# Performance work log

Measured on AMD Instinct MI355X. Metric: run time of the kernel, lower is better.

The kernel has to match this reference:

```python
import jax, jax.numpy as jnp
import numpy as np


def setup_inputs() -> dict:
    key = jax.random.key(0)
    ks = jax.random.split(key, 8)
    B, S, H = 2, 2048, 2048
    Hq, Hkv, D = 16, 4, H // 16
    s = 0.02
    return {
        "query": jax.random.normal(ks[0], (B, S, H), jnp.float32),
        "key": jax.random.normal(ks[1], (B, S, H), jnp.float32),
        "value": jax.random.normal(ks[2], (B, S, H), jnp.float32),
        "Wq": jax.random.normal(ks[3], (H, Hq * D), jnp.float32) * s,
        "bq": jnp.zeros((Hq * D,), jnp.float32),
        "Wk": jax.random.normal(ks[4], (H, Hkv * D), jnp.float32) * s,
        "bk": jnp.zeros((Hkv * D,), jnp.float32),
        "Wv": jax.random.normal(ks[5], (H, Hkv * D), jnp.float32) * s,
        "bv": jnp.zeros((Hkv * D,), jnp.float32),
        "Wo": jax.random.normal(ks[6], (H, H), jnp.float32) * s,
        "bo": jnp.zeros((H,), jnp.float32),
    }


def reference(query, key, value, Wq, bq, Wk, bk, Wv, bv, Wo, bo):
    Hq, Hkv = 16, 4
    B, S, H = query.shape
    D = H // Hq
    G = Hq // Hkv  # heads per KV group
    # projections
    q = query @ Wq + bq   # [B,S,Hq*D]
    k = key @ Wk + bk     # [B,S,Hkv*D]
    v = value @ Wv + bv   # [B,S,Hkv*D]
    # [B, Hkv(groups), G(heads per group), S, D] for q; [B, Hkv, S, D] for k,v
    q = q.reshape(B, S, Hkv, G, D).transpose(0, 2, 3, 1, 4)
    k = k.reshape(B, S, Hkv, D).transpose(0, 2, 1, 3)
    v = v.reshape(B, S, Hkv, D).transpose(0, 2, 1, 3)
    # NOTE: original module applies NO 1/sqrt(D) scaling -- kept faithful.
    attn = jnp.einsum('bghqd,bgkd->bghqk', q, k)  # [B,Hkv,G,S,S]
    attn = jax.nn.softmax(attn, axis=-1)
    out = jnp.einsum('bghqk,bgkd->bghqd', attn, v)  # [B,Hkv,G,S,D]
    # permute(0,3,1,2,4) -> [B,S,Hkv,G,D] -> [B,S,H]
    out = out.transpose(0, 3, 1, 2, 4).reshape(B, S, H)
    return out @ Wo + bo
```

## Files before the change

kernel.cpp:

```cpp
#include <hip/hip_runtime.h>
#include <hip/hip_bf16.h>
#include <type_traits>
#include <stdint.h>

typedef short bf16x8 __attribute__((ext_vector_type(8)));
typedef short short4v __attribute__((ext_vector_type(4)));
typedef float f32x4 __attribute__((ext_vector_type(4)));
typedef float f32x16 __attribute__((ext_vector_type(16)));

#define GLL16(gp, lp) __builtin_amdgcn_global_load_lds( \
    (const __attribute__((address_space(1))) void*)(gp), \
    (__attribute__((address_space(3))) void*)(lp), 16, 0, 0)

__device__ inline short f2bf(float f) {
    union { float f; uint32_t u; } v;
    v.f = f;
    uint32_t r = (v.u + 0x7FFFu + ((v.u >> 16) & 1u)) >> 16;
    return (short)(uint16_t)r;
}

__device__ inline bf16x8 cvt8(const float4& a, const float4& b) {
    bf16x8 o;
    o[0] = f2bf(a.x); o[1] = f2bf(a.y); o[2] = f2bf(a.z); o[3] = f2bf(a.w);
    o[4] = f2bf(b.x); o[5] = f2bf(b.y); o[6] = f2bf(b.z); o[7] = f2bf(b.w);
    return o;
}

__device__ inline uint32_t cvtpk(float lo, float hi) {
    uint32_t r;
    asm("v_cvt_pk_bf16_f32 %0, %1, %2" : "=v"(r) : "v"(lo), "v"(hi));
    return r;
}

__device__ inline bf16x8 mk8(uint32_t a, uint32_t b, uint32_t c, uint32_t d) {
    union { uint32_t u[4]; bf16x8 v; } t;
    t.u[0] = a; t.u[1] = b; t.u[2] = c; t.u[3] = d;
    return t.v;
}

__device__ inline void xchg_pf(const uint32_t c[8], bool hib, bf16x8& fA, bf16x8& fB) {
    uint32_t p0 = (uint32_t)__shfl_xor((int)c[0], 32);
    uint32_t p1 = (uint32_t)__shfl_xor((int)c[1], 32);
    uint32_t p2 = (uint32_t)__shfl_xor((int)c[2], 32);
    uint32_t p3 = (uint32_t)__shfl_xor((int)c[3], 32);
    fA = mk8(hib ? p2 : c[0], hib ? p3 : c[1], hib ? c[2] : p0, hib ? c[3] : p1);
    uint32_t p4 = (uint32_t)__shfl_xor((int)c[4], 32);
    uint32_t p5 = (uint32_t)__shfl_xor((int)c[5], 32);
    uint32_t p6 = (uint32_t)__shfl_xor((int)c[6], 32);
    uint32_t p7 = (uint32_t)__shfl_xor((int)c[7], 32);
    fB = mk8(hib ? p6 : c[4], hib ? p7 : c[5], hib ? c[6] : p4, hib ? c[7] : p5);
}

__global__ __launch_bounds__(256) void prep(
    const float* __restrict__ Wq, const float* __restrict__ Wk,
    const float* __restrict__ Wv, const float* __restrict__ Wo,
    short* __restrict__ WqT, short* __restrict__ WkT,
    short* __restrict__ WvT, short* __restrict__ WoT,
    const float* __restrict__ q, const float* __restrict__ k, const float* __restrict__ v,
    short* __restrict__ Xq, short* __restrict__ Xk, short* __restrict__ Xv)
{
    __shared__ short Tt[64][65];
    const int K = 2048;
    int bid = blockIdx.x;
    int t = threadIdx.x;
    if (bid < 2560) {
        const float* W; short* T; int N; int l;
        if (bid < 1024)      { W = Wq; T = WqT; N = 2048; l = bid; }
        else if (bid < 1280) { W = Wk; T = WkT; N = 512;  l = bid - 1024; }
        else if (bid < 1536) { W = Wv; T = WvT; N = 512;  l = bid - 1280; }
        else                 { W = Wo; T = WoT; N = 2048; l = bid - 1536; }
        int nt = N >> 6;
        int n0 = (l % nt) * 64, k0 = (l / nt) * 64;
        int kl = t >> 2, nb = (t & 3) * 16;
        const float* wp = W + (size_t)(k0 + kl) * N + n0 + nb;
        #pragma unroll
        for (int j = 0; j < 16; ++j) Tt[nb + j][kl] = f2bf(wp[j]);
        __syncthreads();
        int nl = t >> 2, kb = (t & 3) * 16;
        short* op = T + (size_t)(n0 + nl) * K + k0 + kb;
        #pragma unroll
        for (int j = 0; j < 16; ++j) op[j] = Tt[nl][kb + j];
    } else {
        size_t tid = (size_t)(bid - 2560) * 256 + t;
        #pragma unroll
        for (int it = 0; it < 2; ++it) {
            size_t i = tid + (size_t)it * 524288;
            const float4* p;
            p = (const float4*)(q + i * 8);
            *(bf16x8*)(Xq + i * 8) = cvt8(p[0], p[1]);
            p = (const float4*)(k + i * 8);
            *(bf16x8*)(Xk + i * 8) = cvt8(p[0], p[1]);
            p = (const float4*)(v + i * 8);
            *(bf16x8*)(Xv + i * 8) = cvt8(p[0], p[1]);
        }
    }
}

__global__ __launch_bounds__(256) void cvtk(const float* __restrict__ in,
                                            short* __restrict__ out, int n8)
{
    int i = blockIdx.x * blockDim.x + threadIdx.x;
    int stride = gridDim.x * blockDim.x;
    for (; i < n8; i += stride) {
        const float4* p = (const float4*)(in + (size_t)i * 8);
        *(bf16x8*)(out + (size_t)i * 8) = cvt8(p[0], p[1]);
    }
}

__global__ __launch_bounds__(256) void transW4(
    const float* __restrict__ W0, const float* __restrict__ W1,
    const float* __restrict__ W2, const float* __restrict__ W3,
    short* __restrict__ T0, short* __restrict__ T1,
    short* __restrict__ T2, short* __restrict__ T3)
{
    const int K = 2048;
    const float* W; short* T; int N;
    int z = blockIdx.z;
    if (z == 0)      { W = W0; T = T0; N = 2048; }
    else if (z == 1) { W = W1; T = T1; N = 512; }
    else if (z == 2) { W = W2; T = T2; N = 512; }
    else             { W = W3; T = T3; N = 2048; }
    int n0 = blockIdx.x * 64, k0 = blockIdx.y * 64;
    if (n0 >= N) return;
    __shared__ short Tt[64][65];
    int t = threadIdx.x;
    int kl = t >> 2, nb = (t & 3) * 16;
    const float* wp = W + (size_t)(k0 + kl) * N + n0 + nb;
    #pragma unroll
    for (int j = 0; j < 16; ++j) Tt[nb + j][kl] = f2bf(wp[j]);
    __syncthreads();
    int nl = t >> 2, kb = (t & 3) * 16;
    short* op = T + (size_t)(n0 + nl) * K + k0 + kb;
    #pragma unroll
    for (int j = 0; j < 16; ++j) op[j] = Tt[nl][kb + j];
}

__global__ __launch_bounds__(256) void transV(const short* __restrict__ Vb,
                                              short* __restrict__ Vt)
{
    __shared__ short T[64][65];
    int s0 = blockIdx.x * 64, d0 = blockIdx.y * 64, bg = blockIdx.z;
    int b = bg >> 2, g = bg & 3;
    int t = threadIdx.x;
    int sl = t >> 2, db = (t & 3) * 16;
    const short* vp = Vb + (size_t)(b * 2048 + s0 + sl) * 512 + g * 128 + d0 + db;
    #pragma unroll
    for (int j = 0; j < 16; ++j) T[db + j][sl] = vp[j];
    __syncthreads();
    int dl = t >> 2, sb = (t & 3) * 16;
    short* op = Vt + (size_t)(bg * 128 + d0 + dl) * 2048 + s0 + sb;
    #pragma unroll
    for (int j = 0; j < 16; ++j) op[j] = T[dl][sb + j];
}

template <typename TC>
__device__ __forceinline__ void gemm_core(
    const short* __restrict__ A, const short* __restrict__ BT,
    const float* __restrict__ bias, TC* __restrict__ C,
    int N, int K, int m0, int n0, short* As, short* Bs, int epi)
{
    const int t = threadIdx.x, w = t >> 6, lane = t & 63;
    const int lr = lane & 15, lg = lane >> 4;
    const int wm = (w >> 1) * 64, wn = (w & 1) * 64;
    f32x4 acc[4][4] = {};

    const int lrow = lane >> 3;
    const int lcg = (lane & 7) ^ (lrow & 7);
    const int sw = lr & 7;

    const short* abase[2]; const short* bbase[2];
    #pragma unroll
    for (int kc = 0; kc < 2; ++kc) {
        abase[kc] = &As[(wm + lr) * 64 + (((kc * 4 + lg) ^ sw) * 8)];
        bbase[kc] = &Bs[(wn + lr) * 64 + (((kc * 4 + lg) ^ sw) * 8)];
    }
    const short* asrc = A  + (size_t)(m0 + w * 32 + lrow) * K + lcg * 8;
    const short* bsrc = BT + (size_t)(n0 + w * 32 + lrow) * K + lcg * 8;
    short* adst = &As[(w * 32) * 64];
    short* bdst = &Bs[(w * 32) * 64];

    for (int kk = 0; kk < K; kk += 64) {
        __syncthreads();
        #pragma unroll
        for (int i = 0; i < 4; ++i) {
            GLL16(asrc + (size_t)i * 8 * K, adst + i * 512);
            GLL16(bsrc + (size_t)i * 8 * K, bdst + i * 512);
        }
        asrc += 64; bsrc += 64;
        __syncthreads();
        #pragma unroll
        for (int kc = 0; kc < 2; ++kc) {
            bf16x8 af[4], bfr[4];
            #pragma unroll
            for (int i = 0; i < 4; ++i) af[i] = *(const bf16x8*)(abase[kc] + i * 1024);
            #pragma unroll
            for (int j = 0; j < 4; ++j) bfr[j] = *(const bf16x8*)(bbase[kc] + j * 1024);
            #pragma unroll
            for (int i = 0; i < 4; ++i)
                #pragma unroll
                for (int j = 0; j < 4; ++j)
                    acc[i][j] = __builtin_amdgcn_mfma_f32_16x16x32_bf16(af[i], bfr[j], acc[i][j], 0, 0, 0);
        }
    }

    if constexpr (std::is_same<TC, short>::value) {
        if (epi == 1) {
            #pragma unroll
            for (int i = 0; i < 4; ++i) {
                #pragma unroll
                for (int j = 0; j < 4; ++j) {
                    int row = m0 + wm + i * 16 + lg * 4;
                    int col = n0 + wn + j * 16 + lr;
                    short4v s4;
                    #pragma unroll
                    for (int r = 0; r < 4; ++r) s4[r] = f2bf(acc[i][j][r] + bias[col]);
                    int bb = row >> 11, ss = row & 2047;
                    *(short4v*)((short*)C + ((size_t)(bb * 4 + (col >> 7)) * 128 + (col & 127)) * 2048 + ss) = s4;
                }
            }
            return;
        }
    }
    #pragma unroll
    for (int i = 0; i < 4; ++i) {
        #pragma unroll
        for (int j = 0; j < 4; ++j) {
            #pragma unroll
            for (int r = 0; r < 4; ++r) {
                int row = m0 + wm + i * 16 + lg * 4 + r;
                int col = n0 + wn + j * 16 + lr;
                float v = acc[i][j][r] + bias[col];
                if constexpr (std::is_same<TC, short>::value)
                    C[(size_t)row * N + col] = f2bf(v);
                else
                    C[(size_t)row * N + col] = v;
            }
        }
    }
}

template <typename TC>
__global__ __launch_bounds__(256) void gemm_std(
    const short* __restrict__ A, const short* __restrict__ BT,
    const float* __restrict__ bias, TC* __restrict__ C, int N, int K)
{
    __shared__ short As[128 * 64];
    __shared__ short Bs[128 * 64];
    int bid = blockIdx.x;
    int chunk = gridDim.x >> 3;
    int wg = (bid & 7) * chunk + (bid >> 3);
    int m0 = (wg & 31) * 128, n0 = (wg >> 5) * 128;
    gemm_core<TC>(A, BT, bias, C, N, K, m0, n0, As, Bs, 0);
}

__global__ __launch_bounds__(256) void gemm_qkv(
    const short* __restrict__ Xq, const short* __restrict__ Xk, const short* __restrict__ Xv,
    const short* __restrict__ WqT, const short* __restrict__ WkT, const short* __restrict__ WvT,
    const float* __restrict__ bq, const float* __restrict__ bk, const float* __restrict__ bv,
    short* __restrict__ Qb, short* __restrict__ Kb, short* __restrict__ Vt)
{
    __shared__ short As[128 * 64];
    __shared__ short Bs[128 * 64];
    int bid = blockIdx.x;
    int wg = (bid & 7) * 96 + (bid >> 3);
    const short* A; const short* BT; const float* bi; short* C; int N; int l; int epi;
    if (wg < 512)      { l = wg;       A = Xq; BT = WqT; bi = bq; C = Qb; N = 2048; epi = 0; }
    else if (wg < 640) { l = wg - 512; A = Xk; BT = WkT; bi = bk; C = Kb; N = 512;  epi = 0; }
    else               { l = wg - 640; A = Xv; BT = WvT; bi = bv; C = Vt; N = 512;  epi = 1; }
    int m0 = (l & 31) * 128, n0 = (l >> 5) * 128;
    gemm_core<short>(A, BT, bi, C, N, 2048, m0, n0, As, Bs, epi);
}

__global__ __launch_bounds__(512, 2) void attn_kernel(
    const short* __restrict__ Qb, const short* __restrict__ Kb,
    const short* __restrict__ Vt, short* __restrict__ Ob)
{
    const int S = 2048;
    __shared__ short Ks[2 * 64 * 128];
    __shared__ short Vs[2 * 128 * 64];

    int bid = blockIdx.x;
    int wg = (bid & 7) * 32 + (bid >> 3);
    const int qt = wg & 7, bh = wg >> 3;
    const int b = bh >> 4, h = bh & 15, g = h >> 2, bg = b * 4 + g;

    const int t = threadIdx.x, w = t >> 6, lane = t & 63;
    const int l5 = lane & 31, hi = lane >> 5;
    const bool hib = hi != 0;
    const int qg = b * S + qt * 256 + w * 32 + l5;
    const float C = 1.44269504089f;

    const short* qrow = Qb + (size_t)qg * 2048 + h * 128 + hi * 8;
    bf16x8 qf[8];
    #pragma unroll
    for (int dm = 0; dm < 8; ++dm)
        qf[dm] = *(const bf16x8*)(qrow + dm * 16);

    f32x16 o[4] = {};
    float m = -1e30f, l = 0.0f;

    const int sr4 = lane >> 4, sc4 = lane & 15;
    const int sr8 = lane >> 3, sc8 = lane & 7;
    const short* ksrc[2]; const short* vsrc[2];
    #pragma unroll
    for (int i = 0; i < 2; ++i) {
        int kr = w * 8 + i * 4 + sr4;
        ksrc[i] = Kb + (size_t)(b * S + kr) * 512 + g * 128 + ((sc4 ^ (kr & 15)) * 8);
        int d = w * 16 + i * 8 + sr8;
        vsrc[i] = Vt + (size_t)(bg * 128 + d) * 2048 + ((sc8 ^ (d & 7)) * 8);
    }

    int kx[8];
    #pragma unroll
    for (int dm = 0; dm < 8; ++dm)
        kx[dm] = (((dm * 2 + hi) ^ (l5 & 15)) * 8);
    int va[4];
    #pragma unroll
    for (int j = 0; j < 4; ++j)
        va[j] = (((2 * j + hi) ^ (l5 & 7)) * 8);

    #define STAGE(BUF, KVI) do { \
        short* kd = Ks + (BUF) * 8192 + (w * 8) * 128; \
        short* vd = Vs + (BUF) * 8192 + (w * 16) * 64; \
        size_t ko = (size_t)(KVI) * 64 * 512; \
        int vo = (KVI) * 64; \
        _Pragma("unroll") \
        for (int i = 0; i < 2; ++i) { \
            GLL16(ksrc[i] + ko, kd + i * 512); \
            GLL16(vsrc[i] + vo, vd + i * 512); \
        } \
    } while (0)

    STAGE(0, 0);
    const int NT = S / 64;
    for (int ti = 0; ti < NT; ++ti) {
        int cur = ti & 1;
        __syncthreads();
        if (ti + 1 < NT) STAGE(cur ^ 1, ti + 1);

        const short* KB = Ks + cur * 8192 + l5 * 128;
        f32x16 p0 = {}, p1 = {};
        __builtin_amdgcn_s_setprio(1);
        #pragma unroll
        for (int dm = 0; dm < 8; ++dm) {
            bf16x8 k0 = *(const bf16x8*)(KB + kx[dm]);
            bf16x8 k1 = *(const bf16x8*)(KB + 4096 + kx[dm]);
            p0 = __builtin_amdgcn_mfma_f32_32x32x16_bf16(k0, qf[dm], p0, 0, 0, 0);
            p1 = __builtin_amdgcn_mfma_f32_32x32x16_bf16(k1, qf[dm], p1, 0, 0, 0);
        }
        __builtin_amdgcn_s_setprio(0);

        float mx = -1e30f;
        #pragma unroll
        for (int e = 0; e < 16; ++e) mx = fmaxf(mx, fmaxf(p0[e], p1[e]));
        mx = fmaxf(mx, __shfl_xor(mx, 32));
        if (__any(mx > m)) {
            float mn = fmaxf(m, mx);
            float sf = exp2f((m - mn) * C);
            m = mn; l *= sf;
            #pragma unroll
            for (int dblk = 0; dblk < 4; ++dblk)
                #pragma unroll
                for (int e = 0; e < 16; ++e) o[dblk][e] *= sf;
        }
        float nmc = -m * C;
        #pragma unroll
        for (int e = 0; e < 16; ++e) {
            p0[e] = exp2f(fmaf(p0[e], C, nmc));
            p1[e] = exp2f(fmaf(p1[e], C, nmc));
        }
        float rs = 0.0f;
        #pragma unroll
        for (int e = 0; e < 16; ++e) rs += p0[e] + p1[e];
        rs += __shfl_xor(rs, 32);
        l += rs;

        uint32_t c0[8], c1[8];
        #pragma unroll
        for (int i = 0; i < 8; ++i) {
            c0[i] = cvtpk(p0[2 * i], p0[2 * i + 1]);
            c1[i] = cvtpk(p1[2 * i], p1[2 * i + 1]);
        }
        bf16x8 pf[4];
        xchg_pf(c0, hib, pf[0], pf[1]);
        xchg_pf(c1, hib, pf[2], pf[3]);

        const short* VB = Vs + cur * 8192 + l5 * 64;
        __builtin_amdgcn_s_setprio(1);
        #pragma unroll
        for (int dblk = 0; dblk < 4; ++dblk) {
            const short* vb = VB + dblk * 2048;
            #pragma unroll
            for (int j = 0; j < 4; ++j) {
                bf16x8 vf = *(const bf16x8*)(vb + va[j]);
                o[dblk] = __builtin_amdgcn_mfma_f32_32x32x16_bf16(vf, pf[j], o[dblk], 0, 0, 0);
            }
        }
        __builtin_amdgcn_s_setprio(0);
    }
    #undef STAGE

    float inv = 1.0f / l;
    short* op = Ob + (size_t)qg * 2048 + h * 128 + hi * 4;
    #pragma unroll
    for (int dblk = 0; dblk < 4; ++dblk) {
        #pragma unroll
        for (int mm = 0; mm < 4; ++mm) {
            short4v s4;
            #pragma unroll
            for (int e = 0; e < 4; ++e) s4[e] = f2bf(o[dblk][mm * 4 + e] * inv);
            *(short4v*)(op + dblk * 32 + mm * 8) = s4;
        }
    }
}

extern "C" void kernel_launch(void* const* d_in, const int* in_sizes, int n_in,
                              void* d_out, int out_size, void* d_ws, size_t ws_size,
                              hipStream_t stream)
{
    const float* query = (const float*)d_in[0];
    const float* key   = (const float*)d_in[1];
    const float* value = (const float*)d_in[2];
    const float* Wq    = (const float*)d_in[3];
    const float* bq    = (const float*)d_in[4];
    const float* Wk    = (const float*)d_in[5];
    const float* bk    = (const float*)d_in[6];
    const float* Wv    = (const float*)d_in[7];
    const float* bv    = (const float*)d_in[8];
    const float* Wo    = (const float*)d_in[9];
    const float* bo    = (const float*)d_in[10];
    float* out = (float*)d_out;

    const int BS = 4096;
    char* ws = (char*)d_ws;
    dim3 blk(256);
    const size_t MB = 1048576;

    if (ws_size >= 96 * MB) {
        short* Xq  = (short*)(ws + 0);
        short* Xk  = (short*)(ws + 16 * MB);
        short* Xv  = (short*)(ws + 32 * MB);
        short* Qb  = (short*)(ws + 48 * MB);
        short* Kb  = (short*)(ws + 64 * MB);
        short* Vtg = (short*)(ws + 72 * MB);
        short* WqT = (short*)(ws + 76 * MB);
        short* WkT = (short*)(ws + 84 * MB);
        short* WvT = (short*)(ws + 86 * MB);
        short* WoT = (short*)(ws + 88 * MB);
        short* Ob  = Xq;

        prep<<<4608, blk, 0, stream>>>(Wq, Wk, Wv, Wo, WqT, WkT, WvT, WoT,
                                       query, key, value, Xq, Xk, Xv);
        gemm_qkv<<<768, blk, 0, stream>>>(Xq, Xk, Xv, WqT, WkT, WvT, bq, bk, bv, Qb, Kb, Vtg);
        attn_kernel<<<256, dim3(512), 0, stream>>>(Qb, Kb, Vtg, Ob);
        gemm_std<float><<<512, blk, 0, stream>>>(Ob, WoT, bo, out, 2048, 2048);
    } else {
        short* Qb  = (short*)(ws + 0);
        short* Kb  = (short*)(ws + 16777216);
        short* Vb  = (short*)(ws + 20971520);
        short* Vtg = (short*)(ws + 25165824);
        short* WqT = (short*)(ws + 29360128);
        short* WkT = (short*)(ws + 37748736);
        short* WvT = (short*)(ws + 39845888);
        short* WoT = (short*)(ws + 41943040);
        short* Xbf = (short*)(ws + 50331648);

        transW4<<<dim3(32, 32, 4), blk, 0, stream>>>(Wq, Wk, Wv, Wo, WqT, WkT, WvT, WoT);
        cvtk<<<2048, blk, 0, stream>>>(query, Xbf, BS * 2048 / 8);
        gemm_std<short><<<512, blk, 0, stream>>>(Xbf, WqT, bq, Qb, 2048, 2048);
        cvtk<<<2048, blk, 0, stream>>>(key, Xbf, BS * 2048 / 8);
        gemm_std<short><<<128, blk, 0, stream>>>(Xbf, WkT, bk, Kb, 512, 2048);
        cvtk<<<2048, blk, 0, stream>>>(value, Xbf, BS * 2048 / 8);
        gemm_std<short><<<128, blk, 0, stream>>>(Xbf, WvT, bv, Vb, 512, 2048);
        transV<<<dim3(32, 2, 8), blk, 0, stream>>>(Vb, Vtg);
        attn_kernel<<<256, dim3(512), 0, stream>>>(Qb, Kb, Vtg, Xbf);
        gemm_std<float><<<512, blk, 0, stream>>>(Xbf, WoT, bo, out, 2048, 2048);
    }
}
```

Before: 261.9 us.

## Fuse fp32-to-bf16 activation conversion into QKV GEMM and restructure attention blocks

The separate activation conversion pass is removed. The QKV GEMM now reads fp32 inputs directly, converting them to bf16 in registers before storing to LDS, which avoids writing and re-reading bf16 copies of the activations. The attention kernel moves from 512-thread blocks with 256 queries to 256-thread blocks with 128 queries and a doubled grid. It also replaces asynchronous double-buffered global-to-LDS loads with register prefetch into a single LDS buffer, which adds an extra barrier per tile and gives up the direct-to-LDS copy path.

```diff
diff --git a/kernel.cpp b/kernel.cpp
--- a/kernel.cpp
+++ b/kernel.cpp
@@ -51,49 +51,32 @@
     fB = mk8(hib ? p6 : c[4], hib ? p7 : c[5], hib ? c[6] : p4, hib ? c[7] : p5);
 }
 
-__global__ __launch_bounds__(256) void prep(
+__global__ __launch_bounds__(256) void prepW(
     const float* __restrict__ Wq, const float* __restrict__ Wk,
     const float* __restrict__ Wv, const float* __restrict__ Wo,
     short* __restrict__ WqT, short* __restrict__ WkT,
-    short* __restrict__ WvT, short* __restrict__ WoT,
-    const float* __restrict__ q, const float* __restrict__ k, const float* __restrict__ v,
-    short* __restrict__ Xq, short* __restrict__ Xk, short* __restrict__ Xv)
+    short* __restrict__ WvT, short* __restrict__ WoT)
 {
     __shared__ short Tt[64][65];
     const int K = 2048;
     int bid = blockIdx.x;
     int t = threadIdx.x;
-    if (bid < 2560) {
-        const float* W; short* T; int N; int l;
-        if (bid < 1024)      { W = Wq; T = WqT; N = 2048; l = bid; }
-        else if (bid < 1280) { W = Wk; T = WkT; N = 512;  l = bid - 1024; }
-        else if (bid < 1536) { W = Wv; T = WvT; N = 512;  l = bid - 1280; }
-        else                 { W = Wo; T = WoT; N = 2048; l = bid - 1536; }
-        int nt = N >> 6;
-        int n0 = (l % nt) * 64, k0 = (l / nt) * 64;
-        int kl = t >> 2, nb = (t & 3) * 16;
-        const float* wp = W + (size_t)(k0 + kl) * N + n0 + nb;
-        #pragma unroll
-        for (int j = 0; j < 16; ++j) Tt[nb + j][kl] = f2bf(wp[j]);
-        __syncthreads();
-        int nl = t >> 2, kb = (t & 3) * 16;
-        short* op = T + (size_t)(n0 + nl) * K + k0 + kb;
-        #pragma unroll
-        for (int j = 0; j < 16; ++j) op[j] = Tt[nl][kb + j];
-    } else {
-        size_t tid = (size_t)(bid - 2560) * 256 + t;
-        #pragma unroll
-        for (int it = 0; it < 2; ++it) {
-            size_t i = tid + (size_t)it * 524288;
-            const float4* p;
-            p = (const float4*)(q + i * 8);
-            *(bf16x8*)(Xq + i * 8) = cvt8(p[0], p[1]);
-            p = (const float4*)(k + i * 8);
-            *(bf16x8*)(Xk + i * 8) = cvt8(p[0], p[1]);
-            p = (const float4*)(v + i * 8);
-            *(bf16x8*)(Xv + i * 8) = cvt8(p[0], p[1]);
-        }
-    }
+    const float* W; short* T; int N; int l;
+    if (bid < 1024)      { W = Wq; T = WqT; N = 2048; l = bid; }
+    else if (bid < 1280) { W = Wk; T = WkT; N = 512;  l = bid - 1024; }
+    else if (bid < 1536) { W = Wv; T = WvT; N = 512;  l = bid - 1280; }
+    else                 { W = Wo; T = WoT; N = 2048; l = bid - 1536; }
+    int nt = N >> 6;
+    int n0 = (l % nt) * 64, k0 = (l / nt) * 64;
+    int kl = t >> 2, nb = (t & 3) * 16;
+    const float* wp = W + (size_t)(k0 + kl) * N + n0 + nb;
+    #pragma unroll
+    for (int j = 0; j < 16; ++j) Tt[nb + j][kl] = f2bf(wp[j]);
+    __syncthreads();
+    int nl = t >> 2, kb = (t & 3) * 16;
+    short* op = T + (size_t)(n0 + nl) * K + k0 + kb;
+    #pragma unroll
+    for (int j = 0; j < 16; ++j) op[j] = Tt[nl][kb + j];
 }
 
 __global__ __launch_bounds__(256) void cvtk(const float* __restrict__ in,
@@ -105,34 +88,6 @@
         const float4* p = (const float4*)(in + (size_t)i * 8);
         *(bf16x8*)(out + (size_t)i * 8) = cvt8(p[0], p[1]);
     }
-}
-
-__global__ __launch_bounds__(256) void transW4(
-    const float* __restrict__ W0, const float* __restrict__ W1,
-    const float* __restrict__ W2, const float* __restrict__ W3,
-    short* __restrict__ T0, short* __restrict__ T1,
-    short* __restrict__ T2, short* __restrict__ T3)
-{
-    const int K = 2048;
-    const float* W; short* T; int N;
-    int z = blockIdx.z;
-    if (z == 0)      { W = W0; T = T0; N = 2048; }
-    else if (z == 1) { W = W1; T = T1; N = 512; }
-    else if (z == 2) { W = W2; T = T2; N = 512; }
-    else             { W = W3; T = T3; N = 2048; }
-    int n0 = blockIdx.x * 64, k0 = blockIdx.y * 64;
-    if (n0 >= N) return;
-    __shared__ short Tt[64][65];
-    int t = threadIdx.x;
-    int kl = t >> 2, nb = (t & 3) * 16;
-    const float* wp = W + (size_t)(k0 + kl) * N + n0 + nb;
-    #pragma unroll
-    for (int j = 0; j < 16; ++j) Tt[nb + j][kl] = f2bf(wp[j]);
-    __syncthreads();
-    int nl = t >> 2, kb = (t & 3) * 16;
-    short* op = T + (size_t)(n0 + nl) * K + k0 + kb;
-    #pragma unroll
-    for (int j = 0; j < 16; ++j) op[j] = Tt[nl][kb + j];
 }
 
 __global__ __launch_bounds__(256) void transV(const short* __restrict__ Vb,
@@ -157,7 +112,7 @@
 __device__ __forceinline__ void gemm_core(
     const short* __restrict__ A, const short* __restrict__ BT,
     const float* __restrict__ bias, TC* __restrict__ C,
-    int N, int K, int m0, int n0, short* As, short* Bs, int epi)
+    int N, int K, int m0, int n0, short* As, short* Bs)
 {
     const int t = threadIdx.x, w = t >> 6, lane = t & 63;
     const int lr = lane & 15, lg = lane >> 4;
@@ -203,24 +158,6 @@
         }
     }
 
-    if constexpr (std::is_same<TC, short>::value) {
-        if (epi == 1) {
-            #pragma unroll
-            for (int i = 0; i < 4; ++i) {
-                #pragma unroll
-                for (int j = 0; j < 4; ++j) {
-                    int row = m0 + wm + i * 16 + lg * 4;
-                    int col = n0 + wn + j * 16 + lr;
-                    short4v s4;
-                    #pragma unroll
-                    for (int r = 0; r < 4; ++r) s4[r] = f2bf(acc[i][j][r] + bias[col]);
-                    int bb = row >> 11, ss = row & 2047;
-                    *(short4v*)((short*)C + ((size_t)(bb * 4 + (col >> 7)) * 128 + (col & 127)) * 2048 + ss) = s4;
-                }
-            }
-            return;
-        }
-    }
     #pragma unroll
     for (int i = 0; i < 4; ++i) {
         #pragma unroll
@@ -250,11 +187,107 @@
     int chunk = gridDim.x >> 3;
     int wg = (bid & 7) * chunk + (bid >> 3);
     int m0 = (wg & 31) * 128, n0 = (wg >> 5) * 128;
-    gemm_core<TC>(A, BT, bias, C, N, K, m0, n0, As, Bs, 0);
-}
-
-__global__ __launch_bounds__(256) void gemm_qkv(
-    const short* __restrict__ Xq, const short* __restrict__ Xk, const short* __restrict__ Xv,
+    gemm_core<TC>(A, BT, bias, C, N, K, m0, n0, As, Bs);
+}
+
+__device__ __forceinline__ void gemm_core_f32(
+    const float* __restrict__ A, const short* __restrict__ BT,
+    const float* __restrict__ bias, short* __restrict__ C,
+    int N, int m0, int n0, short* As, short* Bs, int epi)
+{
+    const int K = 2048;
+    const int t = threadIdx.x, w = t >> 6, lane = t & 63;
+    const int lr = lane & 15, lg = lane >> 4;
+    const int wm = (w >> 1) * 64, wn = (w & 1) * 64;
+    f32x4 acc[4][4] = {};
+
+    const int lrow = lane >> 3;
+    const int lcg = (lane & 7) ^ (lrow & 7);
+    const int sw = lr & 7;
+
+    const short* abase[2]; const short* bbase[2];
+    #pragma unroll
+    for (int kc = 0; kc < 2; ++kc) {
+        abase[kc] = &As[(wm + lr) * 64 + (((kc * 4 + lg) ^ sw) * 8)];
+        bbase[kc] = &Bs[(wn + lr) * 64 + (((kc * 4 + lg) ^ sw) * 8)];
+    }
+    const float* asrc = A  + (size_t)(m0 + w * 32 + lrow) * K + lcg * 8;
+    const short* bsrc = BT + (size_t)(n0 + w * 32 + lrow) * K + lcg * 8;
+    short* adst = &As[(w * 32) * 64];
+    short* bdst = &Bs[(w * 32) * 64];
+
+    float4 ar0[4], ar1[4];
+    #pragma unroll
+    for (int i = 0; i < 4; ++i) {
+        const float4* ap = (const float4*)(asrc + (size_t)i * 8 * K);
+        ar0[i] = ap[0]; ar1[i] = ap[1];
+    }
+
+    for (int kk = 0; kk < K; kk += 64) {
+        __syncthreads();
+        #pragma unroll
+        for (int i = 0; i < 4; ++i)
+            GLL16(bsrc + (size_t)i * 8 * K, bdst + i * 512);
+        bsrc += 64;
+        #pragma unroll
+        for (int i = 0; i < 4; ++i)
+            *(bf16x8*)(adst + i * 512 + lane * 8) = cvt8(ar0[i], ar1[i]);
+        __syncthreads();
+        if (kk + 64 < K) {
+            asrc += 64;
+            #pragma unroll
+            for (int i = 0; i < 4; ++i) {
+                const float4* ap = (const float4*)(asrc + (size_t)i * 8 * K);
+                ar0[i] = ap[0]; ar1[i] = ap[1];
+            }
+        }
+        #pragma unroll
+        for (int kc = 0; kc < 2; ++kc) {
+            bf16x8 af[4], bfr[4];
+            #pragma unroll
+            for (int i = 0; i < 4; ++i) af[i] = *(const bf16x8*)(abase[kc] + i * 1024);
+            #pragma unroll
+            for (int j = 0; j < 4; ++j) bfr[j] = *(const bf16x8*)(bbase[kc] + j * 1024);
+            #pragma unroll
+            for (int i = 0; i < 4; ++i)
+                #pragma unroll
+                for (int j = 0; j < 4; ++j)
+                    acc[i][j] = __builtin_amdgcn_mfma_f32_16x16x32_bf16(af[i], bfr[j], acc[i][j], 0, 0, 0);
+        }
+    }
+
+    if (epi == 1) {
+        #pragma unroll
+        for (int i = 0; i < 4; ++i) {
+            #pragma unroll
+            for (int j = 0; j < 4; ++j) {
+                int row = m0 + wm + i * 16 + lg * 4;
+                int col = n0 + wn + j * 16 + lr;
+                short4v s4;
+                #pragma unroll
+                for (int r = 0; r < 4; ++r) s4[r] = f2bf(acc[i][j][r] + bias[col]);
+                int bb = row >> 11, ss = row & 2047;
+                *(short4v*)(C + ((size_t)(bb * 4 + (col >> 7)) * 128 + (col & 127)) * 2048 + ss) = s4;
+            }
+        }
+        return;
+    }
+    #pragma unroll
+    for (int i = 0; i < 4; ++i) {
+        #pragma unroll
+        for (int j = 0; j < 4; ++j) {
+            #pragma unroll
+            for (int r = 0; r < 4; ++r) {
+                int row = m0 + wm + i * 16 + lg * 4 + r;
+                int col = n0 + wn + j * 16 + lr;
+                C[(size_t)row * N + col] = f2bf(acc[i][j][r] + bias[col]);
+            }
+        }
+    }
+}
+
+__global__ __launch_bounds__(256, 3) void gemm_qkvf(
+    const float* __restrict__ q, const float* __restrict__ k, const float* __restrict__ v,
     const short* __restrict__ WqT, const short* __restrict__ WkT, const short* __restrict__ WvT,
     const float* __restrict__ bq, const float* __restrict__ bk, const float* __restrict__ bv,
     short* __restrict__ Qb, short* __restrict__ Kb, short* __restrict__ Vt)
@@ -263,31 +296,31 @@
     __shared__ short Bs[128 * 64];
     int bid = blockIdx.x;
     int wg = (bid & 7) * 96 + (bid >> 3);
-    const short* A; const short* BT; const float* bi; short* C; int N; int l; int epi;
-    if (wg < 512)      { l = wg;       A = Xq; BT = WqT; bi = bq; C = Qb; N = 2048; epi = 0; }
-    else if (wg < 640) { l = wg - 512; A = Xk; BT = WkT; bi = bk; C = Kb; N = 512;  epi = 0; }
-    else               { l = wg - 640; A = Xv; BT = WvT; bi = bv; C = Vt; N = 512;  epi = 1; }
+    const float* A; const short* BT; const float* bi; short* C; int N; int l; int epi;
+    if (wg < 512)      { l = wg;       A = q; BT = WqT; bi = bq; C = Qb; N = 2048; epi = 0; }
+    else if (wg < 640) { l = wg - 512; A = k; BT = WkT; bi = bk; C = Kb; N = 512;  epi = 0; }
+    else               { l = wg - 640; A = v; BT = WvT; bi = bv; C = Vt; N = 512;  epi = 1; }
     int m0 = (l & 31) * 128, n0 = (l >> 5) * 128;
-    gemm_core<short>(A, BT, bi, C, N, 2048, m0, n0, As, Bs, epi);
-}
-
-__global__ __launch_bounds__(512, 2) void attn_kernel(
+    gemm_core_f32(A, BT, bi, C, N, m0, n0, As, Bs, epi);
+}
+
+__global__ __launch_bounds__(256, 2) void attn_kernel(
     const short* __restrict__ Qb, const short* __restrict__ Kb,
     const short* __restrict__ Vt, short* __restrict__ Ob)
 {
     const int S = 2048;
-    __shared__ short Ks[2 * 64 * 128];
-    __shared__ short Vs[2 * 128 * 64];
+    __shared__ short Ks[64 * 128];
+    __shared__ short Vs[128 * 64];
 
     int bid = blockIdx.x;
-    int wg = (bid & 7) * 32 + (bid >> 3);
-    const int qt = wg & 7, bh = wg >> 3;
+    int wg = (bid & 7) * 64 + (bid >> 3);
+    const int qt = wg & 15, bh = wg >> 4;
     const int b = bh >> 4, h = bh & 15, g = h >> 2, bg = b * 4 + g;
 
     const int t = threadIdx.x, w = t >> 6, lane = t & 63;
     const int l5 = lane & 31, hi = lane >> 5;
     const bool hib = hi != 0;
-    const int qg = b * S + qt * 256 + w * 32 + l5;
+    const int qg = b * S + qt * 128 + w * 32 + l5;
     const float C = 1.44269504089f;
 
     const short* qrow = Qb + (size_t)qg * 2048 + h * 128 + hi * 8;
@@ -301,12 +334,12 @@
 
     const int sr4 = lane >> 4, sc4 = lane & 15;
     const int sr8 = lane >> 3, sc8 = lane & 7;
-    const short* ksrc[2]; const short* vsrc[2];
-    #pragma unroll
-    for (int i = 0; i < 2; ++i) {
-        int kr = w * 8 + i * 4 + sr4;
+    const short* ksrc[4]; const short* vsrc[4];
+    #pragma unroll
+    for (int i = 0; i < 4; ++i) {
+        int kr = w * 16 + i * 4 + sr4;
         ksrc[i] = Kb + (size_t)(b * S + kr) * 512 + g * 128 + ((sc4 ^ (kr & 15)) * 8);
-        int d = w * 16 + i * 8 + sr8;
+        int d = w * 32 + i * 8 + sr8;
         vsrc[i] = Vt + (size_t)(bg * 128 + d) * 2048 + ((sc8 ^ (d & 7)) * 8);
     }
 
@@ -319,26 +352,36 @@
     for (int j = 0; j < 4; ++j)
         va[j] = (((2 * j + hi) ^ (l5 & 7)) * 8);
 
-    #define STAGE(BUF, KVI) do { \
-        short* kd = Ks + (BUF) * 8192 + (w * 8) * 128; \
-        short* vd = Vs + (BUF) * 8192 + (w * 16) * 64; \
-        size_t ko = (size_t)(KVI) * 64 * 512; \
-        int vo = (KVI) * 64; \
-        _Pragma("unroll") \
-        for (int i = 0; i < 2; ++i) { \
-            GLL16(ksrc[i] + ko, kd + i * 512); \
-            GLL16(vsrc[i] + vo, vd + i * 512); \
-        } \
-    } while (0)
-
-    STAGE(0, 0);
+    short* kd = Ks + (w * 16) * 128 + lane * 8;
+    short* vd = Vs + (w * 32) * 64 + lane * 8;
+
+    bf16x8 kreg[4], vreg[4];
+    #pragma unroll
+    for (int i = 0; i < 4; ++i) {
+        kreg[i] = *(const bf16x8*)(ksrc[i]);
+        vreg[i] = *(const bf16x8*)(vsrc[i]);
+    }
+
     const int NT = S / 64;
     for (int ti = 0; ti < NT; ++ti) {
-        int cur = ti & 1;
         __syncthreads();
-        if (ti + 1 < NT) STAGE(cur ^ 1, ti + 1);
-
-        const short* KB = Ks + cur * 8192 + l5 * 128;
+        #pragma unroll
+        for (int i = 0; i < 4; ++i) {
+            *(bf16x8*)(kd + i * 512) = kreg[i];
+            *(bf16x8*)(vd + i * 512) = vreg[i];
+        }
+        __syncthreads();
+        if (ti + 1 < NT) {
+            size_t ko = (size_t)(ti + 1) * 64 * 512;
+            int vo = (ti + 1) * 64;
+            #pragma unroll
+            for (int i = 0; i < 4; ++i) {
+                kreg[i] = *(const bf16x8*)(ksrc[i] + ko);
+                vreg[i] = *(const bf16x8*)(vsrc[i] + vo);
+            }
+        }
+
+        const short* KB = Ks + l5 * 128;
         f32x16 p0 = {}, p1 = {};
         __builtin_amdgcn_s_setprio(1);
         #pragma unroll
@@ -385,7 +428,7 @@
         xchg_pf(c0, hib, pf[0], pf[1]);
         xchg_pf(c1, hib, pf[2], pf[3]);
 
-        const short* VB = Vs + cur * 8192 + l5 * 64;
+        const short* VB = Vs + l5 * 64;
         __builtin_amdgcn_s_setprio(1);
         #pragma unroll
         for (int dblk = 0; dblk < 4; ++dblk) {
@@ -398,7 +441,6 @@
         }
         __builtin_amdgcn_s_setprio(0);
     }
-    #undef STAGE
 
     float inv = 1.0f / l;
     short* op = Ob + (size_t)qg * 2048 + h * 128 + hi * 4;
@@ -436,23 +478,20 @@
     dim3 blk(256);
     const size_t MB = 1048576;
 
-    if (ws_size >= 96 * MB) {
-        short* Xq  = (short*)(ws + 0);
-        short* Xk  = (short*)(ws + 16 * MB);
-        short* Xv  = (short*)(ws + 32 * MB);
-        short* Qb  = (short*)(ws + 48 * MB);
-        short* Kb  = (short*)(ws + 64 * MB);
-        short* Vtg = (short*)(ws + 72 * MB);
-        short* WqT = (short*)(ws + 76 * MB);
-        short* WkT = (short*)(ws + 84 * MB);
-        short* WvT = (short*)(ws + 86 * MB);
-        short* WoT = (short*)(ws + 88 * MB);
-        short* Ob  = Xq;
-
-        prep<<<4608, blk, 0, stream>>>(Wq, Wk, Wv, Wo, WqT, WkT, WvT, WoT,
-                                       query, key, value, Xq, Xk, Xv);
-        gemm_qkv<<<768, blk, 0, stream>>>(Xq, Xk, Xv, WqT, WkT, WvT, bq, bk, bv, Qb, Kb, Vtg);
-        attn_kernel<<<256, dim3(512), 0, stream>>>(Qb, Kb, Vtg, Ob);
+    if (ws_size >= 64 * MB) {
+        short* Qb  = (short*)(ws + 0);
+        short* Kb  = (short*)(ws + 16 * MB);
+        short* Vtg = (short*)(ws + 20 * MB);
+        short* WqT = (short*)(ws + 24 * MB);
+        short* WkT = (short*)(ws + 32 * MB);
+        short* WvT = (short*)(ws + 34 * MB);
+        short* WoT = (short*)(ws + 36 * MB);
+        short* Ob  = (short*)(ws + 44 * MB);
+
+        prepW<<<2560, blk, 0, stream>>>(Wq, Wk, Wv, Wo, WqT, WkT, WvT, WoT);
+        gemm_qkvf<<<768, blk, 0, stream>>>(query, key, value, WqT, WkT, WvT,
+                                           bq, bk, bv, Qb, Kb, Vtg);
+        attn_kernel<<<512, blk, 0, stream>>>(Qb, Kb, Vtg, Ob);
         gemm_std<float><<<512, blk, 0, stream>>>(Ob, WoT, bo, out, 2048, 2048);
     } else {
         short* Qb  = (short*)(ws + 0);
@@ -465,7 +504,7 @@
         short* WoT = (short*)(ws + 41943040);
         short* Xbf = (short*)(ws + 50331648);
 
-        transW4<<<dim3(32, 32, 4), blk, 0, stream>>>(Wq, Wk, Wv, Wo, WqT, WkT, WvT, WoT);
+        prepW<<<2560, blk, 0, stream>>>(Wq, Wk, Wv, Wo, WqT, WkT, WvT, WoT);
         cvtk<<<2048, blk, 0, stream>>>(query, Xbf, BS * 2048 / 8);
         gemm_std<short><<<512, blk, 0, stream>>>(Xbf, WqT, bq, Qb, 2048, 2048);
         cvtk<<<2048, blk, 0, stream>>>(key, Xbf, BS * 2048 / 8);
@@ -473,7 +512,7 @@
         cvtk<<<2048, blk, 0, stream>>>(value, Xbf, BS * 2048 / 8);
         gemm_std<short><<<128, blk, 0, stream>>>(Xbf, WvT, bv, Vb, 512, 2048);
         transV<<<dim3(32, 2, 8), blk, 0, stream>>>(Vb, Vtg);
-        attn_kernel<<<256, dim3(512), 0, stream>>>(Qb, Kb, Vtg, Xbf);
+        attn_kernel<<<512, blk, 0, stream>>>(Qb, Kb, Vtg, Xbf);
         gemm_std<float><<<512, blk, 0, stream>>>(Xbf, WoT, bo, out, 2048, 2048);
     }
 }
```

Result: slower. 269.1 us (+2.7%).

## Shrink attention blocks to 256 threads with register-staged K/V and permlane swap

Applied to the files above, without the earlier changes.

The attention kernel moves from 512-thread blocks over 256 query rows to 256-thread blocks over 128 rows, launching 512 blocks. The double-buffered direct global-to-LDS loads are replaced by single-buffered LDS fed through registers, with the next tile prefetched into registers during compute. The P-fragment exchange uses permlane32_swap when a runtime probe detects its semantics, falling back to shuffles otherwise. The weight-transpose kernel is rewritten as a flat 1D grid with no dead blocks. The trade-off is two barriers per tile and more register pressure, in exchange for higher occupancy and cheaper lane swaps.

```diff
diff --git a/kernel.cpp b/kernel.cpp
--- a/kernel.cpp
+++ b/kernel.cpp
@@ -49,6 +49,21 @@
     uint32_t p6 = (uint32_t)__shfl_xor((int)c[6], 32);
     uint32_t p7 = (uint32_t)__shfl_xor((int)c[7], 32);
     fB = mk8(hib ? p6 : c[4], hib ? p7 : c[5], hib ? c[6] : p4, hib ? c[7] : p5);
+}
+
+__device__ inline int probe_permlane_mode() {
+#if defined(__has_builtin) && __has_builtin(__builtin_amdgcn_permlane32_swap)
+    int lane = (int)(threadIdx.x & 63);
+    int a = lane, b = lane + 1000;
+    auto r = __builtin_amdgcn_permlane32_swap(a, b, false, false);
+    int l0  = __builtin_amdgcn_readfirstlane(r[0]);
+    int l32 = __builtin_amdgcn_readlane(r[0], 32);
+    if (l0 == 0 && l32 == 1000) return 1;
+    if (l0 == 1032 && l32 == 32) return 2;
+    return 0;
+#else
+    return 0;
+#endif
 }
 
 __global__ __launch_bounds__(256) void prep(
@@ -96,6 +111,34 @@
     }
 }
 
+__global__ __launch_bounds__(256) void prepW(
+    const float* __restrict__ Wq, const float* __restrict__ Wk,
+    const float* __restrict__ Wv, const float* __restrict__ Wo,
+    short* __restrict__ WqT, short* __restrict__ WkT,
+    short* __restrict__ WvT, short* __restrict__ WoT)
+{
+    __shared__ short Tt[64][65];
+    const int K = 2048;
+    int bid = blockIdx.x;
+    int t = threadIdx.x;
+    const float* W; short* T; int N; int l;
+    if (bid < 1024)      { W = Wq; T = WqT; N = 2048; l = bid; }
+    else if (bid < 1280) { W = Wk; T = WkT; N = 512;  l = bid - 1024; }
+    else if (bid < 1536) { W = Wv; T = WvT; N = 512;  l = bid - 1280; }
+    else                 { W = Wo; T = WoT; N = 2048; l = bid - 1536; }
+    int nt = N >> 6;
+    int n0 = (l % nt) * 64, k0 = (l / nt) * 64;
+    int kl = t >> 2, nb = (t & 3) * 16;
+    const float* wp = W + (size_t)(k0 + kl) * N + n0 + nb;
+    #pragma unroll
+    for (int j = 0; j < 16; ++j) Tt[nb + j][kl] = f2bf(wp[j]);
+    __syncthreads();
+    int nl = t >> 2, kb = (t & 3) * 16;
+    short* op = T + (size_t)(n0 + nl) * K + k0 + kb;
+    #pragma unroll
+    for (int j = 0; j < 16; ++j) op[j] = Tt[nl][kb + j];
+}
+
 __global__ __launch_bounds__(256) void cvtk(const float* __restrict__ in,
                                             short* __restrict__ out, int n8)
 {
@@ -105,34 +148,6 @@
         const float4* p = (const float4*)(in + (size_t)i * 8);
         *(bf16x8*)(out + (size_t)i * 8) = cvt8(p[0], p[1]);
     }
-}
-
-__global__ __launch_bounds__(256) void transW4(
-    const float* __restrict__ W0, const float* __restrict__ W1,
-    const float* __restrict__ W2, const float* __restrict__ W3,
-    short* __restrict__ T0, short* __restrict__ T1,
-    short* __restrict__ T2, short* __restrict__ T3)
-{
-    const int K = 2048;
-    const float* W; short* T; int N;
-    int z = blockIdx.z;
-    if (z == 0)      { W = W0; T = T0; N = 2048; }
-    else if (z == 1) { W = W1; T = T1; N = 512; }
-    else if (z == 2) { W = W2; T = T2; N = 512; }
-    else             { W = W3; T = T3; N = 2048; }
-    int n0 = blockIdx.x * 64, k0 = blockIdx.y * 64;
-    if (n0 >= N) return;
-    __shared__ short Tt[64][65];
-    int t = threadIdx.x;
-    int kl = t >> 2, nb = (t & 3) * 16;
-    const float* wp = W + (size_t)(k0 + kl) * N + n0 + nb;
-    #pragma unroll
-    for (int j = 0; j < 16; ++j) Tt[nb + j][kl] = f2bf(wp[j]);
-    __syncthreads();
-    int nl = t >> 2, kb = (t & 3) * 16;
-    short* op = T + (size_t)(n0 + nl) * K + k0 + kb;
-    #pragma unroll
-    for (int j = 0; j < 16; ++j) op[j] = Tt[nl][kb + j];
 }
 
 __global__ __launch_bounds__(256) void transV(const short* __restrict__ Vb,
@@ -271,24 +286,26 @@
     gemm_core<short>(A, BT, bi, C, N, 2048, m0, n0, As, Bs, epi);
 }
 
-__global__ __launch_bounds__(512, 2) void attn_kernel(
+__global__ __launch_bounds__(256, 2) void attn_kernel(
     const short* __restrict__ Qb, const short* __restrict__ Kb,
     const short* __restrict__ Vt, short* __restrict__ Ob)
 {
     const int S = 2048;
-    __shared__ short Ks[2 * 64 * 128];
-    __shared__ short Vs[2 * 128 * 64];
+    __shared__ short Ks[64 * 128];
+    __shared__ short Vs[128 * 64];
 
     int bid = blockIdx.x;
-    int wg = (bid & 7) * 32 + (bid >> 3);
-    const int qt = wg & 7, bh = wg >> 3;
+    int wg = (bid & 7) * 64 + (bid >> 3);
+    const int qt = wg & 15, bh = wg >> 4;
     const int b = bh >> 4, h = bh & 15, g = h >> 2, bg = b * 4 + g;
 
     const int t = threadIdx.x, w = t >> 6, lane = t & 63;
     const int l5 = lane & 31, hi = lane >> 5;
     const bool hib = hi != 0;
-    const int qg = b * S + qt * 256 + w * 32 + l5;
+    const int qg = b * S + qt * 128 + w * 32 + l5;
     const float C = 1.44269504089f;
+
+    const int mode = probe_permlane_mode();
 
     const short* qrow = Qb + (size_t)qg * 2048 + h * 128 + hi * 8;
     bf16x8 qf[8];
@@ -301,12 +318,12 @@
 
     const int sr4 = lane >> 4, sc4 = lane & 15;
     const int sr8 = lane >> 3, sc8 = lane & 7;
-    const short* ksrc[2]; const short* vsrc[2];
-    #pragma unroll
-    for (int i = 0; i < 2; ++i) {
-        int kr = w * 8 + i * 4 + sr4;
+    const short* ksrc[4]; const short* vsrc[4];
+    #pragma unroll
+    for (int i = 0; i < 4; ++i) {
+        int kr = w * 16 + i * 4 + sr4;
         ksrc[i] = Kb + (size_t)(b * S + kr) * 512 + g * 128 + ((sc4 ^ (kr & 15)) * 8);
-        int d = w * 16 + i * 8 + sr8;
+        int d = w * 32 + i * 8 + sr8;
         vsrc[i] = Vt + (size_t)(bg * 128 + d) * 2048 + ((sc8 ^ (d & 7)) * 8);
     }
 
@@ -319,26 +336,36 @@
     for (int j = 0; j < 4; ++j)
         va[j] = (((2 * j + hi) ^ (l5 & 7)) * 8);
 
-    #define STAGE(BUF, KVI) do { \
-        short* kd = Ks + (BUF) * 8192 + (w * 8) * 128; \
-        short* vd = Vs + (BUF) * 8192 + (w * 16) * 64; \
-        size_t ko = (size_t)(KVI) * 64 * 512; \
-        int vo = (KVI) * 64; \
-        _Pragma("unroll") \
-        for (int i = 0; i < 2; ++i) { \
-            GLL16(ksrc[i] + ko, kd + i * 512); \
-            GLL16(vsrc[i] + vo, vd + i * 512); \
-        } \
-    } while (0)
-
-    STAGE(0, 0);
+    short* kd = Ks + (w * 16) * 128 + lane * 8;
+    short* vd = Vs + (w * 32) * 64 + lane * 8;
+
+    bf16x8 kreg[4], vreg[4];
+    #pragma unroll
+    for (int i = 0; i < 4; ++i) {
+        kreg[i] = *(const bf16x8*)(ksrc[i]);
+        vreg[i] = *(const bf16x8*)(vsrc[i]);
+    }
+
     const int NT = S / 64;
     for (int ti = 0; ti < NT; ++ti) {
-        int cur = ti & 1;
         __syncthreads();
-        if (ti + 1 < NT) STAGE(cur ^ 1, ti + 1);
-
-        const short* KB = Ks + cur * 8192 + l5 * 128;
+        #pragma unroll
+        for (int i = 0; i < 4; ++i) {
+            *(bf16x8*)(kd + i * 512) = kreg[i];
+            *(bf16x8*)(vd + i * 512) = vreg[i];
+        }
+        __syncthreads();
+        if (ti + 1 < NT) {
+            size_t ko = (size_t)(ti + 1) * 64 * 512;
+            int vo = (ti + 1) * 64;
+            #pragma unroll
+            for (int i = 0; i < 4; ++i) {
+                kreg[i] = *(const bf16x8*)(ksrc[i] + ko);
+                vreg[i] = *(const bf16x8*)(vsrc[i] + vo);
+            }
+        }
+
+        const short* KB = Ks + l5 * 128;
         f32x16 p0 = {}, p1 = {};
         __builtin_amdgcn_s_setprio(1);
         #pragma unroll
@@ -382,10 +409,41 @@
             c1[i] = cvtpk(p1[2 * i], p1[2 * i + 1]);
         }
         bf16x8 pf[4];
-        xchg_pf(c0, hib, pf[0], pf[1]);
-        xchg_pf(c1, hib, pf[2], pf[3]);
-
-        const short* VB = Vs + cur * 8192 + l5 * 64;
+#if defined(__has_builtin) && __has_builtin(__builtin_amdgcn_permlane32_swap)
+        if (mode == 1) {
+            auto a0 = __builtin_amdgcn_permlane32_swap((int)c0[0], (int)c0[2], false, false);
+            auto a1 = __builtin_amdgcn_permlane32_swap((int)c0[1], (int)c0[3], false, false);
+            auto a2 = __builtin_amdgcn_permlane32_swap((int)c0[4], (int)c0[6], false, false);
+            auto a3 = __builtin_amdgcn_permlane32_swap((int)c0[5], (int)c0[7], false, false);
+            pf[0] = mk8((uint32_t)a0[0], (uint32_t)a1[0], (uint32_t)a0[1], (uint32_t)a1[1]);
+            pf[1] = mk8((uint32_t)a2[0], (uint32_t)a3[0], (uint32_t)a2[1], (uint32_t)a3[1]);
+            auto b0 = __builtin_amdgcn_permlane32_swap((int)c1[0], (int)c1[2], false, false);
+            auto b1 = __builtin_amdgcn_permlane32_swap((int)c1[1], (int)c1[3], false, false);
+            auto b2 = __builtin_amdgcn_permlane32_swap((int)c1[4], (int)c1[6], false, false);
+            auto b3 = __builtin_amdgcn_permlane32_swap((int)c1[5], (int)c1[7], false, false);
+            pf[2] = mk8((uint32_t)b0[0], (uint32_t)b1[0], (uint32_t)b0[1], (uint32_t)b1[1]);
+            pf[3] = mk8((uint32_t)b2[0], (uint32_t)b3[0], (uint32_t)b2[1], (uint32_t)b3[1]);
+        } else if (mode == 2) {
+            auto a0 = __builtin_amdgcn_permlane32_swap((int)c0[2], (int)c0[0], false, false);
+            auto a1 = __builtin_amdgcn_permlane32_swap((int)c0[3], (int)c0[1], false, false);
+            auto a2 = __builtin_amdgcn_permlane32_swap((int)c0[6], (int)c0[4], false, false);
+            auto a3 = __builtin_amdgcn_permlane32_swap((int)c0[7], (int)c0[5], false, false);
+            pf[0] = mk8((uint32_t)a0[1], (uint32_t)a1[1], (uint32_t)a0[0], (uint32_t)a1[0]);
+            pf[1] = mk8((uint32_t)a2[1], (uint32_t)a3[1], (uint32_t)a2[0], (uint32_t)a3[0]);
+            auto b0 = __builtin_amdgcn_permlane32_swap((int)c1[2], (int)c1[0], false, false);
+            auto b1 = __builtin_amdgcn_permlane32_swap((int)c1[3], (int)c1[1], false, false);
+            auto b2 = __builtin_amdgcn_permlane32_swap((int)c1[6], (int)c1[4], false, false);
+            auto b3 = __builtin_amdgcn_permlane32_swap((int)c1[7], (int)c1[5], false, false);
+            pf[2] = mk8((uint32_t)b0[1], (uint32_t)b1[1], (uint32_t)b0[0], (uint32_t)b1[0]);
+            pf[3] = mk8((uint32_t)b2[1], (uint32_t)b3[1], (uint32_t)b2[0], (uint32_t)b3[0]);
+        } else
+#endif
+        {
+            xchg_pf(c0, hib, pf[0], pf[1]);
+            xchg_pf(c1, hib, pf[2], pf[3]);
+        }
+
+        const short* VB = Vs + l5 * 64;
         __builtin_amdgcn_s_setprio(1);
         #pragma unroll
         for (int dblk = 0; dblk < 4; ++dblk) {
@@ -398,7 +456,6 @@
         }
         __builtin_amdgcn_s_setprio(0);
     }
-    #undef STAGE
 
     float inv = 1.0f / l;
     short* op = Ob + (size_t)qg * 2048 + h * 128 + hi * 4;
@@ -452,7 +509,7 @@
         prep<<<4608, blk, 0, stream>>>(Wq, Wk, Wv, Wo, WqT, WkT, WvT, WoT,
                                        query, key, value, Xq, Xk, Xv);
         gemm_qkv<<<768, blk, 0, stream>>>(Xq, Xk, Xv, WqT, WkT, WvT, bq, bk, bv, Qb, Kb, Vtg);
-        attn_kernel<<<256, dim3(512), 0, stream>>>(Qb, Kb, Vtg, Ob);
+        attn_kernel<<<512, blk, 0, stream>>>(Qb, Kb, Vtg, Ob);
         gemm_std<float><<<512, blk, 0, stream>>>(Ob, WoT, bo, out, 2048, 2048);
     } else {
         short* Qb  = (short*)(ws + 0);
@@ -465,7 +522,7 @@
         short* WoT = (short*)(ws + 41943040);
         short* Xbf = (short*)(ws + 50331648);
 
-        transW4<<<dim3(32, 32, 4), blk, 0, stream>>>(Wq, Wk, Wv, Wo, WqT, WkT, WvT, WoT);
+        prepW<<<2560, blk, 0, stream>>>(Wq, Wk, Wv, Wo, WqT, WkT, WvT, WoT);
         cvtk<<<2048, blk, 0, stream>>>(query, Xbf, BS * 2048 / 8);
         gemm_std<short><<<512, blk, 0, stream>>>(Xbf, WqT, bq, Qb, 2048, 2048);
         cvtk<<<2048, blk, 0, stream>>>(key, Xbf, BS * 2048 / 8);
@@ -473,7 +530,7 @@
         cvtk<<<2048, blk, 0, stream>>>(value, Xbf, BS * 2048 / 8);
         gemm_std<short><<<128, blk, 0, stream>>>(Xbf, WvT, bv, Vb, 512, 2048);
         transV<<<dim3(32, 2, 8), blk, 0, stream>>>(Vb, Vtg);
-        attn_kernel<<<256, dim3(512), 0, stream>>>(Qb, Kb, Vtg, Xbf);
+        attn_kernel<<<512, blk, 0, stream>>>(Qb, Kb, Vtg, Xbf);
         gemm_std<float><<<512, blk, 0, stream>>>(Xbf, WoT, bo, out, 2048, 2048);
     }
 }
```

New measurement: 256.3 us (median of 2 runs). -2.2%, faster.
